# Optimization experiments

Measured on AMD Instinct MI355X. Metric: run time of the kernel, lower is better.

## Reference

```python
import jax, jax.numpy as jnp
import numpy as np

CAPS_N, DIMS_N, ROUNDS = 10, 16, 3
IN_CAPS_N, IN_DIMS_N = 1152, 8
BATCH = 256
EPS = 1e-7  # keras backend.epsilon()


def squash(x, axis=-1):
    sq = jnp.sum(x * x, axis=axis, keepdims=True)
    return (sq / (1.0 + sq)) * x / jnp.sqrt(sq + EPS)


def setup_inputs() -> dict:
    key = jax.random.key(0)
    k1, k2 = jax.random.split(key)
    inputs = jax.random.normal(k1, (BATCH, IN_CAPS_N, IN_DIMS_N), dtype=jnp.float32)
    # glorot-ish scale for the transform weights
    W = jax.random.normal(k2, (CAPS_N, IN_CAPS_N, DIMS_N, IN_DIMS_N), dtype=jnp.float32) * 0.05
    return {"inputs": inputs, "W": W}


def reference(inputs, W):
    # u_hat[b,j,i,d] = W[j,i] @ inputs[b,i]  (per-pair prediction vectors)
    u_hat = jnp.einsum('jide,bie->bjid', W, inputs)  # [B, caps_n, in_caps_n, dims_n]
    B = inputs.shape[0]
    cc = jnp.zeros((B, CAPS_N, IN_CAPS_N), dtype=u_hat.dtype)  # routing logits
    v = None
    for r in range(ROUNDS):
        c = jax.nn.softmax(cc, axis=1)                    # softmax over output capsules
        s = jnp.einsum('bji,bjid->bjd', c, u_hat)         # weighted sum over input caps
        v = squash(s, axis=-1)                            # [B, caps_n, dims_n]
        if r != ROUNDS - 1:
            cc = cc + jnp.einsum('bjid,bjd->bji', u_hat, v)  # agreement
    return v
```

## Files before the change

### kernel.cpp

```cpp
#include <hip/hip_runtime.h>

#define B_N 256
#define IC_N 1152
#define J_N 10
#define D_N 16

typedef __attribute__((ext_vector_type(8))) short short8;
typedef __attribute__((ext_vector_type(4))) float floatx4;

union u4s8 { uint4 u; short8 s; };

__device__ __forceinline__ float bf_lo(unsigned int u){
  union { unsigned int i; float f; } c; c.i = u << 16; return c.f;
}
__device__ __forceinline__ float bf_hi(unsigned int u){
  union { unsigned int i; float f; } c; c.i = u & 0xffff0000u; return c.f;
}
__device__ __forceinline__ unsigned int rne16(float f){
  union { float ff; unsigned int i; } c; c.ff = f;
  return (c.i + 0x7FFFu + ((c.i >> 16) & 1u)) >> 16;
}
__device__ __forceinline__ unsigned int pack_rne(float lo, float hi){
  return rne16(lo) | (rne16(hi) << 16);
}
__device__ __forceinline__ unsigned int pack_trunc(float lo, float hi){
  union { float f; unsigned int u; } a, b; a.f = lo; b.f = hi;
  return __builtin_amdgcn_perm(b.u, a.u, 0x07060302u);
}

__global__ __launch_bounds__(256) void caps_prep(
    const float* __restrict__ W, uint4* __restrict__ wsf,
    uint4* __restrict__ wcc2, float* __restrict__ vsum)
{
  const int tid = threadIdx.x;
  const int t0 = blockIdx.x * 256 + tid;
  if (t0 < B_N * J_N * D_N) vsum[t0] = 0.f;
  __shared__ unsigned int lw[1024];
  const int j = blockIdx.x / 72, itile = blockIdx.x % 72;
  const float4* Wt = (const float4*)(W + ((size_t)(j * IC_N + itile * 16) << 7));
  #pragma unroll
  for (int h = 0; h < 2; ++h) {
    const float4 f = Wt[h * 256 + tid];
    lw[(h * 256 + tid) * 2]     = pack_rne(f.x, f.y);
    lw[(h * 256 + tid) * 2 + 1] = pack_rne(f.z, f.w);
  }
  __syncthreads();
  {
    const int ktl = tid >> 6, ln = tid & 63;
    const int base = (ktl * 4 + (ln >> 4)) * 64 + (ln & 15) * 4;
    uint4 q;
    q.x = lw[base]; q.y = lw[base + 1]; q.z = lw[base + 2]; q.w = lw[base + 3];
    wsf[((size_t)j * 288 + itile * 4 + ktl) * 64 + ln] = q;
  }
  {
    const int e = tid >> 5, lane2 = tid & 31;
    const int il = lane2 & 15, dbase = (lane2 >> 4) * 8;
    unsigned short h[8];
    #pragma unroll
    for (int k = 0; k < 8; ++k) {
      const unsigned int u = lw[il * 64 + (dbase + k) * 4 + (e >> 1)];
      h[k] = (e & 1) ? (unsigned short)(u >> 16) : (unsigned short)(u & 0xffffu);
    }
    uint4 q;
    q.x = h[0] | ((unsigned int)h[1] << 16);
    q.y = h[2] | ((unsigned int)h[3] << 16);
    q.z = h[4] | ((unsigned int)h[5] << 16);
    q.w = h[6] | ((unsigned int)h[7] << 16);
    wcc2[(((size_t)j * 8 + e) * 72 + itile) * 32 + lane2] = q;
  }
}

__global__ __launch_bounds__(640, 5) void caps_pass(
    const float* __restrict__ x,
    const uint4* __restrict__ wsf, const uint4* __restrict__ wcc2,
    const uint4* __restrict__ vsbf, float* __restrict__ s_part, const int round)
{
  __shared__ float ccl[10 * 16 * 17];
  __shared__ unsigned int xt[16 * 17 * 4];

  const int tid  = threadIdx.x;
  const int wave = tid >> 6;
  const int lane = tid & 63;
  const int quad = lane >> 4;
  const int col  = lane & 15;
  const int b0   = blockIdx.x << 4;
  const int i0   = blockIdx.y << 4;

  if (tid < 512) {
    const int b = tid >> 5, j4 = tid & 31;
    const int i = j4 >> 1, half = j4 & 1;
    const float4 v = ((const float4*)(x + ((size_t)((b0 + b) * IC_N + i0 + i) << 3)))[half];
    const int idx = ((i * 17 + b) << 2) + (half << 1);
    xt[idx]     = pack_rne(v.x, v.y);
    xt[idx + 1] = pack_rne(v.z, v.w);
  }
  __syncthreads();
  const uint4* xtq = (const uint4*)xt;

  if (round > 0) {
    short8 av = {0,0,0,0,0,0,0,0};
    if (quad < 2)
      av = *(const short8*)&vsbf[((size_t)(b0 + col) * J_N + wave) * 2 + quad];
    uint4 bvq[8];
    #pragma unroll
    for (int e = 0; e < 8; ++e) {
      uint4 q = {0u, 0u, 0u, 0u};
      if (lane < 32)
        q = wcc2[(((size_t)wave * 8 + e) * 72 + blockIdx.y) * 32 + lane];
      bvq[e] = q;
    }
    uint4 xr[4];
    #pragma unroll
    for (int r = 0; r < 4; ++r)
      xr[r] = xtq[col * 17 + quad * 4 + r];
    floatx4 cc4 = {0.f, 0.f, 0.f, 0.f};
    #pragma unroll
    for (int e = 0; e < 8; ++e) {
      u4s8 bv; bv.u = bvq[e];
      floatx4 tf = {0.f, 0.f, 0.f, 0.f};
      tf = __builtin_amdgcn_mfma_f32_16x16x32_bf16(av, bv.s, tf, 0, 0, 0);
      #pragma unroll
      for (int r = 0; r < 4; ++r) {
        const unsigned int u = ((const unsigned int*)&xr[r])[e >> 1];
        const float xe = (e & 1) ? bf_hi(u) : bf_lo(u);
        cc4[r] += tf[r] * xe;
      }
    }
    #pragma unroll
    for (int r = 0; r < 4; ++r)
      ccl[(wave * 16 + col) * 17 + quad * 4 + r] = cc4[r];
    __syncthreads();
    if (tid < 256) {
      const int i = tid >> 4, b = tid & 15;
      float cc[10];
      #pragma unroll
      for (int j = 0; j < 10; ++j) cc[j] = ccl[(j * 16 + i) * 17 + b];
      float m = cc[0];
      #pragma unroll
      for (int j = 1; j < 10; ++j) m = fmaxf(m, cc[j]);
      float den = 0.f;
      #pragma unroll
      for (int j = 0; j < 10; ++j) { cc[j] = __expf(cc[j] - m); den += cc[j]; }
      const float rd = __builtin_amdgcn_rcpf(den);
      #pragma unroll
      for (int j = 0; j < 10; ++j) ccl[(j * 16 + i) * 17 + b] = cc[j] * rd;
    }
    __syncthreads();
  }

  floatx4 acc = {0.f, 0.f, 0.f, 0.f};
  #pragma unroll
  for (int kt = 0; kt < 4; ++kt) {
    const int il = kt * 4 + quad;
    const uint4 xq = xtq[il * 17 + col];
    const uint4 wf = wsf[((size_t)wave * 288 + (blockIdx.y << 2) + kt) * 64 + lane];
    const float c = (round > 0) ? ccl[(wave * 16 + il) * 17 + col] : 0.1f;
    short8 af;
    unsigned int* aq = (unsigned int*)&af;
    aq[0] = pack_trunc(bf_lo(xq.x) * c, bf_hi(xq.x) * c);
    aq[1] = pack_trunc(bf_lo(xq.y) * c, bf_hi(xq.y) * c);
    aq[2] = pack_trunc(bf_lo(xq.z) * c, bf_hi(xq.z) * c);
    aq[3] = pack_trunc(bf_lo(xq.w) * c, bf_hi(xq.w) * c);
    u4s8 bw; bw.u = wf;
    acc = __builtin_amdgcn_mfma_f32_16x16x32_bf16(af, bw.s, acc, 0, 0, 0);
  }
  float* sp = s_part + ((((size_t)blockIdx.x * 10 + wave) * 16 + quad * 4) * 72
                        + blockIdx.y) * 16 + col;
  #pragma unroll
  for (int r = 0; r < 4; ++r) sp[(size_t)r * 72 * 16] = acc[r];
}

__global__ __launch_bounds__(256) void caps_squash(
    const float* __restrict__ s_part, float* __restrict__ vsum,
    unsigned int* __restrict__ vsbf_u, float* __restrict__ out, const int round)
{
  const int tid  = threadIdx.x;
  const int w    = tid >> 6;
  const int lane = tid & 63;
  const int bj   = blockIdx.x * 4 + w;
  const int b    = bj / 10, j = bj - b * 10;
  const int btile = b >> 4, brem = b & 15;
  const float* base = s_part + (((size_t)btile * 10 + j) * 16 + brem) * 1152;
  float acc = 0.f;
  #pragma unroll
  for (int q = 0; q < 18; ++q) acc += base[q * 64 + lane];
  acc += __shfl_xor(acc, 16, 64);
  acc += __shfl_xor(acc, 32, 64);
  const float s = acc;
  float sq = s * s;
  sq += __shfl_xor(sq, 1, 16);
  sq += __shfl_xor(sq, 2, 16);
  sq += __shfl_xor(sq, 4, 16);
  sq += __shfl_xor(sq, 8, 16);
  const float coef = (sq / (1.f + sq)) * rsqrtf(sq + 1e-7f);
  const float v = coef * s;
  if (round < 2) {
    const float vprev = (lane < 16) ? vsum[bj * 16 + lane] : 0.f;
    const float vt = vprev + v;
    const float vtn = __shfl_down(vt, 1, 64);
    if (lane < 16) {
      vsum[bj * 16 + lane] = vt;
      if (!(lane & 1))
        vsbf_u[bj * 8 + (lane >> 1)] = pack_rne(vt, vtn);
    }
  } else if (lane < 16) {
    out[bj * 16 + lane] = v;
  }
}

extern "C" void kernel_launch(void* const* d_in, const int* in_sizes, int n_in,
                              void* d_out, int out_size, void* d_ws, size_t ws_size,
                              hipStream_t stream)
{
  const float* x_p = (const float*)d_in[0];
  const float* W_p = (const float*)d_in[1];

  uint4* wsf   = (uint4*)d_ws;
  uint4* wcc2  = wsf + 184320;
  float* s_prt = (float*)(wcc2 + 184320);
  float* vsum  = s_prt + 2949120;
  unsigned int* vsbf_u = (unsigned int*)(vsum + 40960);
  float* out_p = (float*)d_out;

  caps_prep<<<dim3(720), dim3(256), 0, stream>>>(W_p, wsf, wcc2, vsum);
  for (int r = 0; r < 3; ++r) {
    caps_pass<<<dim3(16, 72), dim3(640), 0, stream>>>(
        x_p, wsf, wcc2, (const uint4*)vsbf_u, s_prt, r);
    caps_squash<<<dim3(640), dim3(256), 0, stream>>>(
        s_prt, vsum, vsbf_u, out_p, r);
  }
}
```

Before: 115.8 us.

## Fuse prep, routing passes and squash into one cooperative persistent kernel

```diff
diff --git a/kernel.cpp b/kernel.cpp
--- a/kernel.cpp
+++ b/kernel.cpp
@@ -1,4 +1,7 @@
 #include <hip/hip_runtime.h>
+#include <hip/hip_cooperative_groups.h>
+
+namespace cg = cooperative_groups;
 
 #define B_N 256
 #define IC_N 1152
@@ -28,183 +31,204 @@
   return __builtin_amdgcn_perm(b.u, a.u, 0x07060302u);
 }
 
-__global__ __launch_bounds__(256) void caps_prep(
-    const float* __restrict__ W, uint4* __restrict__ wsf,
-    uint4* __restrict__ wcc2, float* __restrict__ vsum)
+__global__ __launch_bounds__(640, 5) void caps_fused(
+    const float* __restrict__ x, const float* __restrict__ W,
+    uint4* __restrict__ wsf, uint4* __restrict__ wcc2,
+    float* __restrict__ s_part, float* __restrict__ vsum,
+    unsigned int* __restrict__ vsbf_u, float* __restrict__ out)
 {
-  const int tid = threadIdx.x;
-  const int t0 = blockIdx.x * 256 + tid;
-  if (t0 < B_N * J_N * D_N) vsum[t0] = 0.f;
-  __shared__ unsigned int lw[1024];
-  const int j = blockIdx.x / 72, itile = blockIdx.x % 72;
-  const float4* Wt = (const float4*)(W + ((size_t)(j * IC_N + itile * 16) << 7));
-  #pragma unroll
-  for (int h = 0; h < 2; ++h) {
-    const float4 f = Wt[h * 256 + tid];
-    lw[(h * 256 + tid) * 2]     = pack_rne(f.x, f.y);
-    lw[(h * 256 + tid) * 2 + 1] = pack_rne(f.z, f.w);
-  }
-  __syncthreads();
-  {
-    const int ktl = tid >> 6, ln = tid & 63;
-    const int base = (ktl * 4 + (ln >> 4)) * 64 + (ln & 15) * 4;
-    uint4 q;
-    q.x = lw[base]; q.y = lw[base + 1]; q.z = lw[base + 2]; q.w = lw[base + 3];
-    wsf[((size_t)j * 288 + itile * 4 + ktl) * 64 + ln] = q;
-  }
-  {
-    const int e = tid >> 5, lane2 = tid & 31;
-    const int il = lane2 & 15, dbase = (lane2 >> 4) * 8;
-    unsigned short h[8];
-    #pragma unroll
-    for (int k = 0; k < 8; ++k) {
-      const unsigned int u = lw[il * 64 + (dbase + k) * 4 + (e >> 1)];
-      h[k] = (e & 1) ? (unsigned short)(u >> 16) : (unsigned short)(u & 0xffffu);
-    }
-    uint4 q;
-    q.x = h[0] | ((unsigned int)h[1] << 16);
-    q.y = h[2] | ((unsigned int)h[3] << 16);
-    q.z = h[4] | ((unsigned int)h[5] << 16);
-    q.w = h[6] | ((unsigned int)h[7] << 16);
-    wcc2[(((size_t)j * 8 + e) * 72 + itile) * 32 + lane2] = q;
-  }
-}
-
-__global__ __launch_bounds__(640, 5) void caps_pass(
-    const float* __restrict__ x,
-    const uint4* __restrict__ wsf, const uint4* __restrict__ wcc2,
-    const uint4* __restrict__ vsbf, float* __restrict__ s_part, const int round)
-{
+  cg::grid_group grid = cg::this_grid();
+  const int tid  = threadIdx.x;
+  const int blk  = blockIdx.x;
+  const int nblk = gridDim.x;
+
+  __shared__ unsigned int lw2[2][1024];
   __shared__ float ccl[10 * 16 * 17];
   __shared__ unsigned int xt[16 * 17 * 4];
-
-  const int tid  = threadIdx.x;
+  const uint4* xtq = (const uint4*)xt;
+
+  for (int g = blk * 640 + tid; g < B_N * J_N * D_N; g += nblk * 640)
+    vsum[g] = 0.f;
+
+  {
+    const int grp = tid >> 8;
+    const int p   = tid & 255;
+    for (int base = 0; base < 720; base += nblk * 2) {
+      const int pvb = base + blk * 2 + grp;
+      const bool act = (grp < 2) && (pvb < 720);
+      unsigned int* lw = lw2[grp & 1];
+      const int j = pvb / 72, itile = pvb % 72;
+      if (act) {
+        const float4* Wt = (const float4*)(W + ((size_t)(j * IC_N + itile * 16) << 7));
+        #pragma unroll
+        for (int h = 0; h < 2; ++h) {
+          const float4 f = Wt[h * 256 + p];
+          lw[(h * 256 + p) * 2]     = pack_rne(f.x, f.y);
+          lw[(h * 256 + p) * 2 + 1] = pack_rne(f.z, f.w);
+        }
+      }
+      __syncthreads();
+      if (act) {
+        {
+          const int ktl = p >> 6, ln = p & 63;
+          const int fb = (ktl * 4 + (ln >> 4)) * 64 + (ln & 15) * 4;
+          uint4 q;
+          q.x = lw[fb]; q.y = lw[fb + 1]; q.z = lw[fb + 2]; q.w = lw[fb + 3];
+          wsf[((size_t)j * 288 + itile * 4 + ktl) * 64 + ln] = q;
+        }
+        {
+          const int e = p >> 5, lane2 = p & 31;
+          const int il = lane2 & 15, dbase = (lane2 >> 4) * 8;
+          unsigned short h[8];
+          #pragma unroll
+          for (int k = 0; k < 8; ++k) {
+            const unsigned int u = lw[il * 64 + (dbase + k) * 4 + (e >> 1)];
+            h[k] = (e & 1) ? (unsigned short)(u >> 16) : (unsigned short)(u & 0xffffu);
+          }
+          uint4 q;
+          q.x = h[0] | ((unsigned int)h[1] << 16);
+          q.y = h[2] | ((unsigned int)h[3] << 16);
+          q.z = h[4] | ((unsigned int)h[5] << 16);
+          q.w = h[6] | ((unsigned int)h[7] << 16);
+          wcc2[(((size_t)j * 8 + e) * 72 + itile) * 32 + lane2] = q;
+        }
+      }
+      __syncthreads();
+    }
+  }
+
+  grid.sync();
+
   const int wave = tid >> 6;
   const int lane = tid & 63;
   const int quad = lane >> 4;
   const int col  = lane & 15;
-  const int b0   = blockIdx.x << 4;
-  const int i0   = blockIdx.y << 4;
-
-  if (tid < 512) {
-    const int b = tid >> 5, j4 = tid & 31;
-    const int i = j4 >> 1, half = j4 & 1;
-    const float4 v = ((const float4*)(x + ((size_t)((b0 + b) * IC_N + i0 + i) << 3)))[half];
-    const int idx = ((i * 17 + b) << 2) + (half << 1);
-    xt[idx]     = pack_rne(v.x, v.y);
-    xt[idx + 1] = pack_rne(v.z, v.w);
-  }
-  __syncthreads();
-  const uint4* xtq = (const uint4*)xt;
-
-  if (round > 0) {
-    short8 av = {0,0,0,0,0,0,0,0};
-    if (quad < 2)
-      av = *(const short8*)&vsbf[((size_t)(b0 + col) * J_N + wave) * 2 + quad];
-    uint4 bvq[8];
-    #pragma unroll
-    for (int e = 0; e < 8; ++e) {
-      uint4 q = {0u, 0u, 0u, 0u};
-      if (lane < 32)
-        q = wcc2[(((size_t)wave * 8 + e) * 72 + blockIdx.y) * 32 + lane];
-      bvq[e] = q;
+
+  for (int round = 0; round < 3; ++round) {
+    for (int vbid = blk; vbid < 16 * 72; vbid += nblk) {
+      const int bx = vbid & 15;
+      const int by = vbid >> 4;
+      const int b0 = bx << 4;
+      const int i0 = by << 4;
+
+      __syncthreads();
+      if (tid < 512) {
+        const int b = tid >> 5, j4 = tid & 31;
+        const int i = j4 >> 1, half = j4 & 1;
+        const float4 v = ((const float4*)(x + ((size_t)((b0 + b) * IC_N + i0 + i) << 3)))[half];
+        const int idx = ((i * 17 + b) << 2) + (half << 1);
+        xt[idx]     = pack_rne(v.x, v.y);
+        xt[idx + 1] = pack_rne(v.z, v.w);
+      }
+      __syncthreads();
+
+      if (round > 0) {
+        short8 av = {0,0,0,0,0,0,0,0};
+        if (quad < 2)
+          av = *(const short8*)((const uint4*)vsbf_u +
+                                ((size_t)(b0 + col) * J_N + wave) * 2 + quad);
+        uint4 bvq[8];
+        #pragma unroll
+        for (int e = 0; e < 8; ++e) {
+          uint4 q = {0u, 0u, 0u, 0u};
+          if (lane < 32)
+            q = wcc2[(((size_t)wave * 8 + e) * 72 + by) * 32 + lane];
+          bvq[e] = q;
+        }
+        uint4 xr[4];
+        #pragma unroll
+        for (int r = 0; r < 4; ++r)
+          xr[r] = xtq[col * 17 + quad * 4 + r];
+        floatx4 cc4 = {0.f, 0.f, 0.f, 0.f};
+        #pragma unroll
+        for (int e = 0; e < 8; ++e) {
+          u4s8 bv; bv.u = bvq[e];
+          floatx4 tf = {0.f, 0.f, 0.f, 0.f};
+          tf = __builtin_amdgcn_mfma_f32_16x16x32_bf16(av, bv.s, tf, 0, 0, 0);
+          #pragma unroll
+          for (int r = 0; r < 4; ++r) {
+            const unsigned int u = ((const unsigned int*)&xr[r])[e >> 1];
+            const float xe = (e & 1) ? bf_hi(u) : bf_lo(u);
+            cc4[r] += tf[r] * xe;
+          }
+        }
+        #pragma unroll
+        for (int r = 0; r < 4; ++r)
+          ccl[(wave * 16 + col) * 17 + quad * 4 + r] = cc4[r];
+        __syncthreads();
+        if (tid < 256) {
+          const int i = tid >> 4, b = tid & 15;
+          float cc[10];
+          #pragma unroll
+          for (int j = 0; j < 10; ++j) cc[j] = ccl[(j * 16 + i) * 17 + b];
+          float m = cc[0];
+          #pragma unroll
+          for (int j = 1; j < 10; ++j) m = fmaxf(m, cc[j]);
+          float den = 0.f;
+          #pragma unroll
+          for (int j = 0; j < 10; ++j) { cc[j] = __expf(cc[j] - m); den += cc[j]; }
+          const float rd = __builtin_amdgcn_rcpf(den);
+          #pragma unroll
+          for (int j = 0; j < 10; ++j) ccl[(j * 16 + i) * 17 + b] = cc[j] * rd;
+        }
+        __syncthreads();
+      }
+
+      floatx4 acc = {0.f, 0.f, 0.f, 0.f};
+      #pragma unroll
+      for (int kt = 0; kt < 4; ++kt) {
+        const int il = kt * 4 + quad;
+        const uint4 xq = xtq[il * 17 + col];
+        const uint4 wf = wsf[((size_t)wave * 288 + (by << 2) + kt) * 64 + lane];
+        const float c = (round > 0) ? ccl[(wave * 16 + il) * 17 + col] : 0.1f;
+        short8 af;
+        unsigned int* aq = (unsigned int*)&af;
+        aq[0] = pack_trunc(bf_lo(xq.x) * c, bf_hi(xq.x) * c);
+        aq[1] = pack_trunc(bf_lo(xq.y) * c, bf_hi(xq.y) * c);
+        aq[2] = pack_trunc(bf_lo(xq.z) * c, bf_hi(xq.z) * c);
+        aq[3] = pack_trunc(bf_lo(xq.w) * c, bf_hi(xq.w) * c);
+        u4s8 bw; bw.u = wf;
+        acc = __builtin_amdgcn_mfma_f32_16x16x32_bf16(af, bw.s, acc, 0, 0, 0);
+      }
+      float* sp = s_part + ((((size_t)bx * 10 + wave) * 16 + quad * 4) * 72 + by) * 16 + col;
+      #pragma unroll
+      for (int r = 0; r < 4; ++r) sp[(size_t)r * 72 * 16] = acc[r];
     }
-    uint4 xr[4];
-    #pragma unroll
-    for (int r = 0; r < 4; ++r)
-      xr[r] = xtq[col * 17 + quad * 4 + r];
-    floatx4 cc4 = {0.f, 0.f, 0.f, 0.f};
-    #pragma unroll
-    for (int e = 0; e < 8; ++e) {
-      u4s8 bv; bv.u = bvq[e];
-      floatx4 tf = {0.f, 0.f, 0.f, 0.f};
-      tf = __builtin_amdgcn_mfma_f32_16x16x32_bf16(av, bv.s, tf, 0, 0, 0);
+
+    grid.sync();
+
+    for (int bj = blk * 10 + wave; bj < B_N * J_N; bj += nblk * 10) {
+      const int b = bj / 10, j = bj - b * 10;
+      const int btile = b >> 4, brem = b & 15;
+      const float* sbase = s_part + (((size_t)btile * 10 + j) * 16 + brem) * 1152;
+      float acc = 0.f;
       #pragma unroll
-      for (int r = 0; r < 4; ++r) {
-        const unsigned int u = ((const unsigned int*)&xr[r])[e >> 1];
-        const float xe = (e & 1) ? bf_hi(u) : bf_lo(u);
-        cc4[r] += tf[r] * xe;
+      for (int q = 0; q < 18; ++q) acc += sbase[q * 64 + lane];
+      acc += __shfl_xor(acc, 16, 64);
+      acc += __shfl_xor(acc, 32, 64);
+      const float s = acc;
+      float sq = s * s;
+      sq += __shfl_xor(sq, 1, 16);
+      sq += __shfl_xor(sq, 2, 16);
+      sq += __shfl_xor(sq, 4, 16);
+      sq += __shfl_xor(sq, 8, 16);
+      const float coef = (sq / (1.f + sq)) * rsqrtf(sq + 1e-7f);
+      const float v = coef * s;
+      if (round < 2) {
+        const float vprev = (lane < 16) ? vsum[bj * 16 + lane] : 0.f;
+        const float vt = vprev + v;
+        const float vtn = __shfl_down(vt, 1, 64);
+        if (lane < 16) {
+          vsum[bj * 16 + lane] = vt;
+          if (!(lane & 1))
+            vsbf_u[bj * 8 + (lane >> 1)] = pack_rne(vt, vtn);
+        }
+      } else if (lane < 16) {
+        out[bj * 16 + lane] = v;
       }
     }
-    #pragma unroll
-    for (int r = 0; r < 4; ++r)
-      ccl[(wave * 16 + col) * 17 + quad * 4 + r] = cc4[r];
-    __syncthreads();
-    if (tid < 256) {
-      const int i = tid >> 4, b = tid & 15;
-      float cc[10];
-      #pragma unroll
-      for (int j = 0; j < 10; ++j) cc[j] = ccl[(j * 16 + i) * 17 + b];
-      float m = cc[0];
-      #pragma unroll
-      for (int j = 1; j < 10; ++j) m = fmaxf(m, cc[j]);
-      float den = 0.f;
-      #pragma unroll
-      for (int j = 0; j < 10; ++j) { cc[j] = __expf(cc[j] - m); den += cc[j]; }
-      const float rd = __builtin_amdgcn_rcpf(den);
-      #pragma unroll
-      for (int j = 0; j < 10; ++j) ccl[(j * 16 + i) * 17 + b] = cc[j] * rd;
-    }
-    __syncthreads();
-  }
-
-  floatx4 acc = {0.f, 0.f, 0.f, 0.f};
-  #pragma unroll
-  for (int kt = 0; kt < 4; ++kt) {
-    const int il = kt * 4 + quad;
-    const uint4 xq = xtq[il * 17 + col];
-    const uint4 wf = wsf[((size_t)wave * 288 + (blockIdx.y << 2) + kt) * 64 + lane];
-    const float c = (round > 0) ? ccl[(wave * 16 + il) * 17 + col] : 0.1f;
-    short8 af;
-    unsigned int* aq = (unsigned int*)&af;
-    aq[0] = pack_trunc(bf_lo(xq.x) * c, bf_hi(xq.x) * c);
-    aq[1] = pack_trunc(bf_lo(xq.y) * c, bf_hi(xq.y) * c);
-    aq[2] = pack_trunc(bf_lo(xq.z) * c, bf_hi(xq.z) * c);
-    aq[3] = pack_trunc(bf_lo(xq.w) * c, bf_hi(xq.w) * c);
-    u4s8 bw; bw.u = wf;
-    acc = __builtin_amdgcn_mfma_f32_16x16x32_bf16(af, bw.s, acc, 0, 0, 0);
-  }
-  float* sp = s_part + ((((size_t)blockIdx.x * 10 + wave) * 16 + quad * 4) * 72
-                        + blockIdx.y) * 16 + col;
-  #pragma unroll
-  for (int r = 0; r < 4; ++r) sp[(size_t)r * 72 * 16] = acc[r];
-}
-
-__global__ __launch_bounds__(256) void caps_squash(
-    const float* __restrict__ s_part, float* __restrict__ vsum,
-    unsigned int* __restrict__ vsbf_u, float* __restrict__ out, const int round)
-{
-  const int tid  = threadIdx.x;
-  const int w    = tid >> 6;
-  const int lane = tid & 63;
-  const int bj   = blockIdx.x * 4 + w;
-  const int b    = bj / 10, j = bj - b * 10;
-  const int btile = b >> 4, brem = b & 15;
-  const float* base = s_part + (((size_t)btile * 10 + j) * 16 + brem) * 1152;
-  float acc = 0.f;
-  #pragma unroll
-  for (int q = 0; q < 18; ++q) acc += base[q * 64 + lane];
-  acc += __shfl_xor(acc, 16, 64);
-  acc += __shfl_xor(acc, 32, 64);
-  const float s = acc;
-  float sq = s * s;
-  sq += __shfl_xor(sq, 1, 16);
-  sq += __shfl_xor(sq, 2, 16);
-  sq += __shfl_xor(sq, 4, 16);
-  sq += __shfl_xor(sq, 8, 16);
-  const float coef = (sq / (1.f + sq)) * rsqrtf(sq + 1e-7f);
-  const float v = coef * s;
-  if (round < 2) {
-    const float vprev = (lane < 16) ? vsum[bj * 16 + lane] : 0.f;
-    const float vt = vprev + v;
-    const float vtn = __shfl_down(vt, 1, 64);
-    if (lane < 16) {
-      vsum[bj * 16 + lane] = vt;
-      if (!(lane & 1))
-        vsbf_u[bj * 8 + (lane >> 1)] = pack_rne(vt, vtn);
-    }
-  } else if (lane < 16) {
-    out[bj * 16 + lane] = v;
+
+    if (round < 2) grid.sync();
   }
 }
 
@@ -222,11 +246,19 @@
   unsigned int* vsbf_u = (unsigned int*)(vsum + 40960);
   float* out_p = (float*)d_out;
 
-  caps_prep<<<dim3(720), dim3(256), 0, stream>>>(W_p, wsf, wcc2, vsum);
-  for (int r = 0; r < 3; ++r) {
-    caps_pass<<<dim3(16, 72), dim3(640), 0, stream>>>(
-        x_p, wsf, wcc2, (const uint4*)vsbf_u, s_prt, r);
-    caps_squash<<<dim3(640), dim3(256), 0, stream>>>(
-        s_prt, vsum, vsbf_u, out_p, r);
+  static int s_grid = 0;
+  if (s_grid == 0) {
+    int occ = 0;
+    hipError_t err = hipOccupancyMaxActiveBlocksPerMultiprocessor(
+        &occ, (const void*)caps_fused, 640, 0);
+    if (err != hipSuccess || occ < 1) occ = 1;
+    long g = (long)occ * 256;
+    if (g > 512) g = 512;
+    s_grid = (int)g;
   }
-}
+
+  void* args[] = {(void*)&x_p, (void*)&W_p, (void*)&wsf, (void*)&wcc2,
+                  (void*)&s_prt, (void*)&vsum, (void*)&vsbf_u, (void*)&out_p};
+  hipLaunchCooperativeKernel((const void*)caps_fused, dim3(s_grid), dim3(640),
+                             args, 0, stream);
+}
```

After: 317.9 us. 174% more time.

## Collapse caps_pass to one wave per tile looping over all output capsules

Applied to the files above, without the earlier changes.

```diff
diff --git a/kernel.cpp b/kernel.cpp
--- a/kernel.cpp
+++ b/kernel.cpp
@@ -70,7 +70,7 @@
   }
 }
 
-__global__ __launch_bounds__(640, 5) void caps_pass(
+__global__ __launch_bounds__(64, 3) void caps_pass(
     const float* __restrict__ x,
     const uint4* __restrict__ wsf, const uint4* __restrict__ wcc2,
     const uint4* __restrict__ vsbf, float* __restrict__ s_part, const int round)
@@ -78,96 +78,126 @@
   __shared__ float ccl[10 * 16 * 17];
   __shared__ unsigned int xt[16 * 17 * 4];
 
-  const int tid  = threadIdx.x;
-  const int wave = tid >> 6;
-  const int lane = tid & 63;
+  const int lane = threadIdx.x;
   const int quad = lane >> 4;
   const int col  = lane & 15;
-  const int b0   = blockIdx.x << 4;
-  const int i0   = blockIdx.y << 4;
-
-  if (tid < 512) {
-    const int b = tid >> 5, j4 = tid & 31;
-    const int i = j4 >> 1, half = j4 & 1;
+
+  const int bid = blockIdx.x;
+  const int wid = (bid & 7) * 144 + (bid >> 3);
+  const int bx  = wid & 15;
+  const int by  = wid >> 4;
+  const int b0  = bx << 4;
+  const int i0  = by << 4;
+
+  #pragma unroll
+  for (int t = 0; t < 8; ++t) {
+    const int idx = t * 64 + lane;
+    const int b = idx >> 5, i4 = idx & 31;
+    const int i = i4 >> 1, half = i4 & 1;
     const float4 v = ((const float4*)(x + ((size_t)((b0 + b) * IC_N + i0 + i) << 3)))[half];
-    const int idx = ((i * 17 + b) << 2) + (half << 1);
-    xt[idx]     = pack_rne(v.x, v.y);
-    xt[idx + 1] = pack_rne(v.z, v.w);
+    const int o = ((i * 17 + b) << 2) + (half << 1);
+    xt[o]     = pack_rne(v.x, v.y);
+    xt[o + 1] = pack_rne(v.z, v.w);
   }
   __syncthreads();
   const uint4* xtq = (const uint4*)xt;
 
   if (round > 0) {
-    short8 av = {0,0,0,0,0,0,0,0};
-    if (quad < 2)
-      av = *(const short8*)&vsbf[((size_t)(b0 + col) * J_N + wave) * 2 + quad];
-    uint4 bvq[8];
-    #pragma unroll
-    for (int e = 0; e < 8; ++e) {
-      uint4 q = {0u, 0u, 0u, 0u};
-      if (lane < 32)
-        q = wcc2[(((size_t)wave * 8 + e) * 72 + blockIdx.y) * 32 + lane];
-      bvq[e] = q;
-    }
     uint4 xr[4];
     #pragma unroll
     for (int r = 0; r < 4; ++r)
       xr[r] = xtq[col * 17 + quad * 4 + r];
-    floatx4 cc4 = {0.f, 0.f, 0.f, 0.f};
-    #pragma unroll
-    for (int e = 0; e < 8; ++e) {
-      u4s8 bv; bv.u = bvq[e];
-      floatx4 tf = {0.f, 0.f, 0.f, 0.f};
-      tf = __builtin_amdgcn_mfma_f32_16x16x32_bf16(av, bv.s, tf, 0, 0, 0);
-      #pragma unroll
-      for (int r = 0; r < 4; ++r) {
-        const unsigned int u = ((const unsigned int*)&xr[r])[e >> 1];
-        const float xe = (e & 1) ? bf_hi(u) : bf_lo(u);
-        cc4[r] += tf[r] * xe;
+    floatx4 cc4[10];
+    #pragma unroll
+    for (int j = 0; j < 10; ++j) {
+      short8 av = {0,0,0,0,0,0,0,0};
+      if (quad < 2)
+        av = *(const short8*)&vsbf[((size_t)(b0 + col) * J_N + j) * 2 + quad];
+      floatx4 c4 = {0.f, 0.f, 0.f, 0.f};
+      #pragma unroll
+      for (int e = 0; e < 8; ++e) {
+        uint4 q = {0u, 0u, 0u, 0u};
+        if (lane < 32)
+          q = wcc2[(((size_t)j * 8 + e) * 72 + by) * 32 + lane];
+        u4s8 bv; bv.u = q;
+        floatx4 tf = {0.f, 0.f, 0.f, 0.f};
+        tf = __builtin_amdgcn_mfma_f32_16x16x32_bf16(av, bv.s, tf, 0, 0, 0);
+        #pragma unroll
+        for (int r = 0; r < 4; ++r) {
+          const unsigned int u = ((const unsigned int*)&xr[r])[e >> 1];
+          const float xe = (e & 1) ? bf_hi(u) : bf_lo(u);
+          c4[r] += tf[r] * xe;
+        }
       }
-    }
-    #pragma unroll
-    for (int r = 0; r < 4; ++r)
-      ccl[(wave * 16 + col) * 17 + quad * 4 + r] = cc4[r];
+      cc4[j] = c4;
+    }
+    #pragma unroll
+    for (int r = 0; r < 4; ++r) {
+      float m = cc4[0][r];
+      #pragma unroll
+      for (int j = 1; j < 10; ++j) m = fmaxf(m, cc4[j][r]);
+      float e10[10];
+      float den = 0.f;
+      #pragma unroll
+      for (int j = 0; j < 10; ++j) { e10[j] = __expf(cc4[j][r] - m); den += e10[j]; }
+      const float rd = __builtin_amdgcn_rcpf(den);
+      #pragma unroll
+      for (int j = 0; j < 10; ++j)
+        ccl[(j * 16 + col) * 17 + quad * 4 + r] = e10[j] * rd;
+    }
     __syncthreads();
-    if (tid < 256) {
-      const int i = tid >> 4, b = tid & 15;
-      float cc[10];
-      #pragma unroll
-      for (int j = 0; j < 10; ++j) cc[j] = ccl[(j * 16 + i) * 17 + b];
-      float m = cc[0];
-      #pragma unroll
-      for (int j = 1; j < 10; ++j) m = fmaxf(m, cc[j]);
-      float den = 0.f;
-      #pragma unroll
-      for (int j = 0; j < 10; ++j) { cc[j] = __expf(cc[j] - m); den += cc[j]; }
-      const float rd = __builtin_amdgcn_rcpf(den);
-      #pragma unroll
-      for (int j = 0; j < 10; ++j) ccl[(j * 16 + i) * 17 + b] = cc[j] * rd;
-    }
-    __syncthreads();
-  }
-
-  floatx4 acc = {0.f, 0.f, 0.f, 0.f};
-  #pragma unroll
-  for (int kt = 0; kt < 4; ++kt) {
-    const int il = kt * 4 + quad;
-    const uint4 xq = xtq[il * 17 + col];
-    const uint4 wf = wsf[((size_t)wave * 288 + (blockIdx.y << 2) + kt) * 64 + lane];
-    const float c = (round > 0) ? ccl[(wave * 16 + il) * 17 + col] : 0.1f;
-    short8 af;
-    unsigned int* aq = (unsigned int*)&af;
-    aq[0] = pack_trunc(bf_lo(xq.x) * c, bf_hi(xq.x) * c);
-    aq[1] = pack_trunc(bf_lo(xq.y) * c, bf_hi(xq.y) * c);
-    aq[2] = pack_trunc(bf_lo(xq.z) * c, bf_hi(xq.z) * c);
-    aq[3] = pack_trunc(bf_lo(xq.w) * c, bf_hi(xq.w) * c);
-    u4s8 bw; bw.u = wf;
-    acc = __builtin_amdgcn_mfma_f32_16x16x32_bf16(af, bw.s, acc, 0, 0, 0);
-  }
-  float* sp = s_part + ((((size_t)blockIdx.x * 10 + wave) * 16 + quad * 4) * 72
-                        + blockIdx.y) * 16 + col;
-  #pragma unroll
-  for (int r = 0; r < 4; ++r) sp[(size_t)r * 72 * 16] = acc[r];
+  }
+
+  uint4 xq[4];
+  #pragma unroll
+  for (int kt = 0; kt < 4; ++kt)
+    xq[kt] = xtq[(kt * 4 + quad) * 17 + col];
+
+  if (round == 0) {
+    short8 af4[4];
+    #pragma unroll
+    for (int kt = 0; kt < 4; ++kt) {
+      unsigned int* aq = (unsigned int*)&af4[kt];
+      const uint4 q = xq[kt];
+      aq[0] = pack_trunc(bf_lo(q.x) * 0.1f, bf_hi(q.x) * 0.1f);
+      aq[1] = pack_trunc(bf_lo(q.y) * 0.1f, bf_hi(q.y) * 0.1f);
+      aq[2] = pack_trunc(bf_lo(q.z) * 0.1f, bf_hi(q.z) * 0.1f);
+      aq[3] = pack_trunc(bf_lo(q.w) * 0.1f, bf_hi(q.w) * 0.1f);
+    }
+    #pragma unroll
+    for (int j = 0; j < 10; ++j) {
+      floatx4 acc = {0.f, 0.f, 0.f, 0.f};
+      #pragma unroll
+      for (int kt = 0; kt < 4; ++kt) {
+        u4s8 bw; bw.u = wsf[((size_t)j * 288 + (by << 2) + kt) * 64 + lane];
+        acc = __builtin_amdgcn_mfma_f32_16x16x32_bf16(af4[kt], bw.s, acc, 0, 0, 0);
+      }
+      float* sp = s_part + ((((size_t)bx * 10 + j) * 16 + quad * 4) * 72 + by) * 16 + col;
+      #pragma unroll
+      for (int r = 0; r < 4; ++r) sp[(size_t)r * 72 * 16] = acc[r];
+    }
+  } else {
+    #pragma unroll
+    for (int j = 0; j < 10; ++j) {
+      floatx4 acc = {0.f, 0.f, 0.f, 0.f};
+      #pragma unroll
+      for (int kt = 0; kt < 4; ++kt) {
+        const float c = ccl[(j * 16 + (kt * 4 + quad)) * 17 + col];
+        const uint4 q = xq[kt];
+        short8 af;
+        unsigned int* aq = (unsigned int*)&af;
+        aq[0] = pack_trunc(bf_lo(q.x) * c, bf_hi(q.x) * c);
+        aq[1] = pack_trunc(bf_lo(q.y) * c, bf_hi(q.y) * c);
+        aq[2] = pack_trunc(bf_lo(q.z) * c, bf_hi(q.z) * c);
+        aq[3] = pack_trunc(bf_lo(q.w) * c, bf_hi(q.w) * c);
+        u4s8 bw; bw.u = wsf[((size_t)j * 288 + (by << 2) + kt) * 64 + lane];
+        acc = __builtin_amdgcn_mfma_f32_16x16x32_bf16(af, bw.s, acc, 0, 0, 0);
+      }
+      float* sp = s_part + ((((size_t)bx * 10 + j) * 16 + quad * 4) * 72 + by) * 16 + col;
+      #pragma unroll
+      for (int r = 0; r < 4; ++r) sp[(size_t)r * 72 * 16] = acc[r];
+    }
+  }
 }
 
 __global__ __launch_bounds__(256) void caps_squash(
@@ -224,7 +254,7 @@
 
   caps_prep<<<dim3(720), dim3(256), 0, stream>>>(W_p, wsf, wcc2, vsum);
   for (int r = 0; r < 3; ++r) {
-    caps_pass<<<dim3(16, 72), dim3(640), 0, stream>>>(
+    caps_pass<<<dim3(1152), dim3(64), 0, stream>>>(
         x_p, wsf, wcc2, (const uint4*)vsbf_u, s_prt, r);
     caps_squash<<<dim3(640), dim3(256), 0, stream>>>(
         s_prt, vsum, vsbf_u, out_p, r);
```

After: 182.8 us. +57.8%, slower.
